# Optimization experiments

Measured on AMD Instinct MI355X. Metric: run time of the kernel, lower is better.

The kernel has to match this reference:

```python
import jax, jax.numpy as jnp
import numpy as np

DIM = 768
HEADS = 12
HIDDEN = int(DIM * 4.0)


def layernorm(x, w, b, eps=1e-5):
    mu = jnp.mean(x, axis=-1, keepdims=True)
    var = jnp.var(x, axis=-1, keepdims=True)
    return (x - mu) * jax.lax.rsqrt(var + eps) * w + b


def setup_inputs() -> dict:
    key = jax.random.key(0)
    ks = jax.random.split(key, 16)
    B, Nq, Nc, D = 4, 1024, 1024, DIM
    s = 0.02
    return {
        "query_tokens": jax.random.normal(ks[0], (B, Nq, D), jnp.float32),
        "context_tokens": jax.random.normal(ks[1], (B, Nc, D), jnp.float32),
        "wind_bias": jax.random.normal(ks[2], (B, 1, Nq, Nc), jnp.float32),
        "ln_q_w": jnp.ones((D,), jnp.float32), "ln_q_b": jnp.zeros((D,), jnp.float32),
        "ln_kv_w": jnp.ones((D,), jnp.float32), "ln_kv_b": jnp.zeros((D,), jnp.float32),
        "Wq": jax.random.normal(ks[3], (D, D), jnp.float32) * s, "bq": jnp.zeros((D,), jnp.float32),
        "Wk": jax.random.normal(ks[4], (D, D), jnp.float32) * s, "bk": jnp.zeros((D,), jnp.float32),
        "Wv": jax.random.normal(ks[5], (D, D), jnp.float32) * s, "bv": jnp.zeros((D,), jnp.float32),
        "Wo": jax.random.normal(ks[6], (D, D), jnp.float32) * s, "bo": jnp.zeros((D,), jnp.float32),
        "beta": jnp.ones((HEADS, 1, 1), jnp.float32),
        "ln_f_w": jnp.ones((D,), jnp.float32), "ln_f_b": jnp.zeros((D,), jnp.float32),
        "W1": jax.random.normal(ks[7], (D, HIDDEN), jnp.float32) * s, "b1": jnp.zeros((HIDDEN,), jnp.float32),
        "W2": jax.random.normal(ks[8], (HIDDEN, D), jnp.float32) * s, "b2": jnp.zeros((D,), jnp.float32),
    }


def reference(query_tokens, context_tokens, wind_bias,
              ln_q_w, ln_q_b, ln_kv_w, ln_kv_b,
              Wq, bq, Wk, bk, Wv, bv, Wo, bo, beta,
              ln_f_w, ln_f_b, W1, b1, W2, b2):
    B, Nq, D = query_tokens.shape
    H = HEADS
    hd = D // H
    scale = hd ** -0.5

    q = layernorm(query_tokens, ln_q_w, ln_q_b) @ Wq + bq
    kv = layernorm(context_tokens, ln_kv_w, ln_kv_b)
    k = kv @ Wk + bk
    v = kv @ Wv + bv

    # [B, H, N, hd]
    q = q.reshape(B, Nq, H, hd).transpose(0, 2, 1, 3)
    k = k.reshape(B, -1, H, hd).transpose(0, 2, 1, 3)
    v = v.reshape(B, -1, H, hd).transpose(0, 2, 1, 3)

    attn = jnp.einsum('bhqd,bhkd->bhqk', q * scale, k)
    attn = attn + beta * wind_bias  # beta: [H,1,1] broadcasts over [B,H,Nq,Nc]
    attn = jax.nn.softmax(attn.astype(jnp.float32), axis=-1).astype(q.dtype)

    out = jnp.einsum('bhqk,bhkd->bhqd', attn, v).transpose(0, 2, 1, 3).reshape(B, Nq, D)
    out = out @ Wo + bo

    x = query_tokens + out
    h = layernorm(x, ln_f_w, ln_f_b)
    h = jax.nn.gelu(h @ W1 + b1, approximate=False) @ W2 + b2
    return x + h
```

## Files before the change

### kernel.cpp

```cpp
#include <hip/hip_runtime.h>
#include <hip/hip_bf16.h>


#define DIM 768
#define HID 3072
#define NHEAD 12
#define BATCH 4
#define SEQ 1024
#define ROWS (BATCH * SEQ)
#define HD 64

typedef __attribute__((ext_vector_type(8))) __bf16 bf16x8;
typedef __attribute__((ext_vector_type(4))) float f32x4;
typedef __attribute__((ext_vector_type(4))) unsigned int u32x4;
typedef __attribute__((ext_vector_type(2))) unsigned int u32x2;

#define MFMA16(a, b, c) __builtin_amdgcn_mfma_f32_16x16x32_bf16((a), (b), (c), 0, 0, 0)

#define GLDS16(g, l)                                                         \
  __builtin_amdgcn_global_load_lds(                                          \
      (const __attribute__((address_space(1))) void*)(g),                    \
      (__attribute__((address_space(3))) void*)(l), 16, 0, 0)

__device__ __forceinline__ unsigned pk2(float lo, float hi) {
  unsigned a = __bfloat16_as_ushort(__float2bfloat16(lo));
  unsigned b = __bfloat16_as_ushort(__float2bfloat16(hi));
  return a | (b << 16);
}

__global__ __launch_bounds__(256) void wg_transpose4(const float* __restrict__ Wq,
                                                     const float* __restrict__ Wk,
                                                     const float* __restrict__ Wv,
                                                     const float* __restrict__ Wo,
                                                     __hip_bfloat16* __restrict__ WqT,
                                                     __hip_bfloat16* __restrict__ WkT,
                                                     __hip_bfloat16* __restrict__ WvT,
                                                     __hip_bfloat16* __restrict__ WoT) {
  __shared__ float tile[32][33];
  const int z = blockIdx.z;
  const float* W = (z == 0) ? Wq : (z == 1) ? Wk : (z == 2) ? Wv : Wo;
  __hip_bfloat16* WT = (z == 0) ? WqT : (z == 1) ? WkT : (z == 2) ? WvT : WoT;
  const int tx = threadIdx.x & 31, ty = threadIdx.x >> 5;
  const int n0 = blockIdx.x * 32, k0 = blockIdx.y * 32;
#pragma unroll
  for (int i = 0; i < 4; i++)
    tile[ty + i * 8][tx] = W[(size_t)(k0 + ty + i * 8) * DIM + n0 + tx];
  __syncthreads();
#pragma unroll
  for (int i = 0; i < 4; i++)
    WT[(size_t)(n0 + ty + i * 8) * DIM + k0 + tx] = __float2bfloat16(tile[tx][ty + i * 8]);
}

__global__ __launch_bounds__(256) void wg_transpose(const float* __restrict__ W,
                                                    __hip_bfloat16* __restrict__ WT,
                                                    int K, int N) {
  __shared__ float tile[32][33];
  const int tx = threadIdx.x & 31, ty = threadIdx.x >> 5;
  const int n0 = blockIdx.x * 32, k0 = blockIdx.y * 32;
#pragma unroll
  for (int i = 0; i < 4; i++)
    tile[ty + i * 8][tx] = W[(size_t)(k0 + ty + i * 8) * N + n0 + tx];
  __syncthreads();
#pragma unroll
  for (int i = 0; i < 4; i++)
    WT[(size_t)(n0 + ty + i * 8) * K + k0 + tx] = __float2bfloat16(tile[tx][ty + i * 8]);
}

__global__ void wg_bcat(const float* __restrict__ bq, const float* __restrict__ bk,
                        const float* __restrict__ bv, float* __restrict__ bc) {
  int i = blockIdx.x * 256 + threadIdx.x;
  if (i < 768) bc[i] = bq[i];
  else if (i < 1536) bc[i] = bk[i - 768];
  else if (i < 2304) bc[i] = bv[i - 1536];
}

template <int DUAL>
__global__ __launch_bounds__(256) void wg_ln(const float* __restrict__ inA,
                                             const float* __restrict__ wA,
                                             const float* __restrict__ bA,
                                             const float* __restrict__ inB,
                                             const float* __restrict__ wB,
                                             const float* __restrict__ bB,
                                             __hip_bfloat16* __restrict__ outbuf) {
  int row = blockIdx.x;
  int t = threadIdx.x;
  const float* in = inA;
  const float* w = wA;
  const float* b = bA;
  int lrow = row;
  if (DUAL && row >= ROWS) {
    in = inB; w = wB; b = bB; lrow = row - ROWS;
  }
  const float* p = in + (size_t)lrow * DIM;
  float v0 = p[t], v1 = p[t + 256], v2 = p[t + 512];
  float s = v0 + v1 + v2;
  float q = v0 * v0 + v1 * v1 + v2 * v2;
#pragma unroll
  for (int d = 1; d < 64; d <<= 1) {
    s += __shfl_xor(s, d);
    q += __shfl_xor(q, d);
  }
  __shared__ float ss[4], sq[4];
  if ((t & 63) == 0) {
    ss[t >> 6] = s;
    sq[t >> 6] = q;
  }
  __syncthreads();
  s = ss[0] + ss[1] + ss[2] + ss[3];
  q = sq[0] + sq[1] + sq[2] + sq[3];
  float mu = s * (1.0f / DIM);
  float var = q * (1.0f / DIM) - mu * mu;
  float rs = rsqrtf(var + 1e-5f);
  __hip_bfloat16* o = outbuf + (size_t)row * DIM;
  o[t] = __float2bfloat16((v0 - mu) * rs * w[t] + b[t]);
  o[t + 256] = __float2bfloat16((v1 - mu) * rs * w[t + 256] + b[t + 256]);
  o[t + 512] = __float2bfloat16((v2 - mu) * rs * w[t + 512] + b[t + 512]);
}

template <int MODE>
__global__ __launch_bounds__(512) void wg_gemm(const __hip_bfloat16* __restrict__ A,
                                               const __hip_bfloat16* __restrict__ BT,
                                               const float* __restrict__ bias,
                                               void* __restrict__ Cout,
                                               const float* __restrict__ resid,
                                               float* __restrict__ aux,
                                               int N, int Kloop, int Kstride, float p0) {
  __shared__ __hip_bfloat16 As[3][128 * 32];
  __shared__ __hip_bfloat16 Bs[3][128 * 32];
  const int t = threadIdx.x;
  const int lane = t & 63;
  const int wave = t >> 6;
  const int wr = wave >> 1, wc = wave & 1;
  const int lhi = lane >> 4, llo = lane & 15;
  const int nbn = N >> 7;
  const int bm = blockIdx.x / nbn, bn = blockIdx.x % nbn;
  const int koff = (MODE == 7) ? blockIdx.y * Kloop : 0;

  const __hip_bfloat16* Ause = A;
  if (MODE == 6 && bn >= 6) Ause = A + (size_t)ROWS * DIM;

  const int srow = t >> 2;
  const int sg = ((t & 3) ^ ((srow >> 1) & 3)) * 8;
  const __hip_bfloat16* Ag = Ause + (size_t)(bm * 128 + srow) * Kstride + koff + sg;
  const __hip_bfloat16* Bg = BT + (size_t)(bn * 128 + srow) * Kstride + koff + sg;

  f32x4 zero = {0.f, 0.f, 0.f, 0.f};
  f32x4 acc[2][4];
#pragma unroll
  for (int i = 0; i < 2; i++)
#pragma unroll
    for (int j = 0; j < 4; j++) acc[i][j] = zero;

  const int nk = Kloop >> 5;

  GLDS16(Ag, &As[0][t * 8]);
  GLDS16(Bg, &Bs[0][t * 8]);
  GLDS16(Ag + 32, &As[1][t * 8]);
  GLDS16(Bg + 32, &Bs[1][t * 8]);

  int buf = 0;
  for (int kt = 0; kt < nk; kt++) {
    if (kt < nk - 1) {
      asm volatile("s_waitcnt vmcnt(2)" ::: "memory");
    } else {
      asm volatile("s_waitcnt vmcnt(0)" ::: "memory");
    }
    __builtin_amdgcn_s_barrier();
    asm volatile("" ::: "memory");
    if (kt + 2 < nk) {
      int nbuf = buf + 2;
      if (nbuf >= 3) nbuf -= 3;
      GLDS16(Ag + (kt + 2) * 32, &As[nbuf][t * 8]);
      GLDS16(Bg + (kt + 2) * 32, &Bs[nbuf][t * 8]);
    }
    bf16x8 af[2], bfr[4];
#pragma unroll
    for (int i = 0; i < 2; i++) {
      const int row = wr * 32 + i * 16 + llo;
      af[i] = *reinterpret_cast<const bf16x8*>(
          &As[buf][row * 32 + ((lhi ^ ((row >> 1) & 3)) << 3)]);
    }
#pragma unroll
    for (int j = 0; j < 4; j++) {
      const int row = wc * 64 + j * 16 + llo;
      bfr[j] = *reinterpret_cast<const bf16x8*>(
          &Bs[buf][row * 32 + ((lhi ^ ((row >> 1) & 3)) << 3)]);
    }
    __builtin_amdgcn_s_setprio(1);
#pragma unroll
    for (int i = 0; i < 2; i++)
#pragma unroll
      for (int j = 0; j < 4; j++) acc[i][j] = MFMA16(af[i], bfr[j], acc[i][j]);
    __builtin_amdgcn_s_setprio(0);
    buf++;
    if (buf == 3) buf = 0;
  }

#pragma unroll
  for (int i = 0; i < 2; i++) {
    int gr = bm * 128 + wr * 32 + i * 16 + lhi * 4;
#pragma unroll
    for (int j = 0; j < 4; j++) {
      int gc = bn * 128 + wc * 64 + j * 16 + llo;
      float bv_ = (MODE == 7) ? 0.f : bias[gc];
#pragma unroll
      for (int r = 0; r < 4; r++) {
        float v = acc[i][j][r] + bv_;
        int row = gr + r;
        size_t idx = (size_t)row * N + gc;
        if (MODE == 3) {
          aux[idx] = resid[idx] + v;
        } else if (MODE == 4) {
          float x3 = v * v * v;
          float z = -2.302208f * v - 0.102943f * x3;
          float g = v / (1.0f + exp2f(z));
          ((__hip_bfloat16*)Cout)[idx] = __float2bfloat16(g);
        } else if (MODE == 7) {
          aux[(size_t)blockIdx.y * ROWS * N + idx] = v;
        } else if (MODE == 6) {
          int sec = gc / 768;
          int n2 = gc - sec * 768;
          __hip_bfloat16* base = (__hip_bfloat16*)Cout;
          if (sec == 0) {
            base[(size_t)row * DIM + n2] = __float2bfloat16(v * p0);
          } else if (sec == 1) {
            base[(size_t)ROWS * DIM + (size_t)row * DIM + n2] = __float2bfloat16(v);
          } else {
            int b_ = row >> 10, n_ = row & 1023;
            int h_ = n2 >> 6, d_ = n2 & 63;
            base[(size_t)2 * ROWS * DIM +
                 (((size_t)(b_ * NHEAD + h_) * HD + d_) << 10) + n_] = __float2bfloat16(v);
          }
        }
      }
    }
  }
}

template <int NP>
__global__ __launch_bounds__(256) void wg_red(const float* __restrict__ partial,
                                              const float* __restrict__ resid,
                                              const float* __restrict__ bias,
                                              float* __restrict__ out) {
  const int i = blockIdx.x * 256 + threadIdx.x;
  const int NF4 = ROWS * DIM / 4;
  if (i >= NF4) return;
  const f32x4* P = (const f32x4*)partial;
  f32x4 p = P[i];
#pragma unroll
  for (int c = 1; c < NP; c++) p += P[i + c * NF4];
  f32x4 r = ((const f32x4*)resid)[i];
  f32x4 bv = ((const f32x4*)bias)[i % (DIM / 4)];
  ((f32x4*)out)[i] = r + p + bv;
}

__global__ __launch_bounds__(256) void wg_attn4(const __hip_bfloat16* __restrict__ Q,
                                                const __hip_bfloat16* __restrict__ Kb,
                                                const __hip_bfloat16* __restrict__ Vt,
                                                const float* __restrict__ wb,
                                                const float* __restrict__ beta,
                                                __hip_bfloat16* __restrict__ O) {
  __shared__ __hip_bfloat16 Ks[2][4096];
  __shared__ __hip_bfloat16 Vs[2][4096];
  const int t = threadIdx.x;
  const int lane = t & 63;
  const int lhi = lane >> 4, llo = lane & 15;

  const int bid = blockIdx.x;
  const int wid = (bid & 7) * 96 + (bid >> 3);
  const int h = wid % NHEAD;
  const int g = wid / NHEAD;
  const int qt = g & 15;
  const int b = g >> 4;
  const float betah = beta[h] * 1.44269504089f;

  const int w = t >> 6;
  const size_t qrow0 = (size_t)b * SEQ + qt * 64 + w * 16;
  const __hip_bfloat16* Qp = Q + qrow0 * DIM + h * HD;
  bf16x8 a0 = *reinterpret_cast<const bf16x8*>(&Qp[(size_t)llo * DIM + lhi * 8]);
  bf16x8 a1 = *reinterpret_cast<const bf16x8*>(&Qp[(size_t)llo * DIM + 32 + lhi * 8]);

  const __hip_bfloat16* Kg = Kb + (size_t)b * SEQ * DIM + h * HD;
  const __hip_bfloat16* Vg = Vt + (size_t)(b * NHEAD + h) * HD * SEQ;
  const float* wrow = wb + (qrow0 + llo) * SEQ;

  const int slot0 = t, slot1 = t + 256;
  const int r0 = slot0 >> 3, c0 = (slot0 & 7) ^ (r0 & 7);
  const int r1 = slot1 >> 3, c1 = (slot1 & 7) ^ (r1 & 7);

  auto stage = [&](int buf, int kb) {
    GLDS16(Kg + (size_t)(kb + r0) * DIM + c0 * 8, &Ks[buf][slot0 * 8]);
    GLDS16(Kg + (size_t)(kb + r1) * DIM + c1 * 8, &Ks[buf][slot1 * 8]);
    GLDS16(Vg + (size_t)r0 * SEQ + kb + c0 * 8, &Vs[buf][slot0 * 8]);
    GLDS16(Vg + (size_t)r1 * SEQ + kb + c1 * 8, &Vs[buf][slot1 * 8]);
  };

  f32x4 zero = {0.f, 0.f, 0.f, 0.f};
  f32x4 oc[4];
#pragma unroll
  for (int c = 0; c < 4; c++) oc[c] = zero;
  float m_ = -1e30f, l_ = 0.f;

  f32x4 wv[4];
#pragma unroll
  for (int c2 = 0; c2 < 4; c2++)
    wv[c2] = *reinterpret_cast<const f32x4*>(&wrow[c2 * 16 + lhi * 4]);

  stage(0, 0);
  __syncthreads();
  int cur = 0;

  const int srcA = (lane & 15) | ((lane & 16) << 1);
  const bool chi = (lane & 32) != 0;

  for (int kt = 0; kt < SEQ / 64; kt++) {
    const int kb = kt * 64;
    f32x4 wvn[4];
    if (kt < SEQ / 64 - 1) {
      stage(cur ^ 1, kb + 64);
#pragma unroll
      for (int c2 = 0; c2 < 4; c2++)
        wvn[c2] = *reinterpret_cast<const f32x4*>(&wrow[kb + 64 + c2 * 16 + lhi * 4]);
    }

    f32x4 sv[4];
    __builtin_amdgcn_s_setprio(1);
#pragma unroll
    for (int c2 = 0; c2 < 4; c2++) {
      const int row = c2 * 16 + llo;
      bf16x8 k0 = *reinterpret_cast<const bf16x8*>(
          &Ks[cur][((row << 3) + (lhi ^ (row & 7))) << 3]);
      bf16x8 k1 = *reinterpret_cast<const bf16x8*>(
          &Ks[cur][((row << 3) + ((4 + lhi) ^ (row & 7))) << 3]);
      f32x4 s_ = zero;
      s_ = MFMA16(k0, a0, s_);
      s_ = MFMA16(k1, a1, s_);
      sv[c2] = s_;
    }
    __builtin_amdgcn_s_setprio(0);

#pragma unroll
    for (int c2 = 0; c2 < 4; c2++)
#pragma unroll
      for (int r = 0; r < 4; r++) sv[c2][r] += betah * wv[c2][r];

    float mx;
    {
      f32x4 m4;
#pragma unroll
      for (int r = 0; r < 4; r++)
        m4[r] = fmaxf(fmaxf(sv[0][r], sv[1][r]), fmaxf(sv[2][r], sv[3][r]));
      mx = fmaxf(fmaxf(m4[0], m4[1]), fmaxf(m4[2], m4[3]));
      mx = fmaxf(mx, __shfl_xor(mx, 16));
      mx = fmaxf(mx, __shfl_xor(mx, 32));
    }

    const bool grow = __any(mx > m_);
    float corr = 1.f;
    if (grow) {
      float mn = fmaxf(m_, mx);
      corr = exp2f(m_ - mn);
      m_ = mn;
    }

#pragma unroll
    for (int c2 = 0; c2 < 4; c2++)
#pragma unroll
      for (int r = 0; r < 4; r++) sv[c2][r] = exp2f(sv[c2][r] - m_);
    f32x4 s4;
#pragma unroll
    for (int r = 0; r < 4; r++) s4[r] = (sv[0][r] + sv[1][r]) + (sv[2][r] + sv[3][r]);
    float rs = (s4[0] + s4[1]) + (s4[2] + s4[3]);
    rs += __shfl_xor(rs, 16);
    rs += __shfl_xor(rs, 32);
    l_ = l_ * corr + rs;

    if (grow) {
      float cr[4];
#pragma unroll
      for (int r = 0; r < 4; r++) cr[r] = __shfl(corr, lhi * 4 + r);
#pragma unroll
      for (int c = 0; c < 4; c++)
#pragma unroll
        for (int r = 0; r < 4; r++) oc[c][r] *= cr[r];
    }

    unsigned p01[4], p23[4];
#pragma unroll
    for (int c2 = 0; c2 < 4; c2++) {
      p01[c2] = pk2(sv[c2][0], sv[c2][1]);
      p23[c2] = pk2(sv[c2][2], sv[c2][3]);
    }
    unsigned a01_0A = (unsigned)__shfl((int)p01[0], srcA);
    unsigned a01_1A = (unsigned)__shfl((int)p01[1], srcA);
    unsigned a23_0A = (unsigned)__shfl((int)p23[0], srcA);
    unsigned a23_1A = (unsigned)__shfl((int)p23[1], srcA);
    unsigned a01_0B = (unsigned)__shfl((int)p01[0], srcA + 16);
    unsigned a01_1B = (unsigned)__shfl((int)p01[1], srcA + 16);
    unsigned a23_0B = (unsigned)__shfl((int)p23[0], srcA + 16);
    unsigned a23_1B = (unsigned)__shfl((int)p23[1], srcA + 16);
    unsigned b01_2A = (unsigned)__shfl((int)p01[2], srcA);
    unsigned b01_3A = (unsigned)__shfl((int)p01[3], srcA);
    unsigned b23_2A = (unsigned)__shfl((int)p23[2], srcA);
    unsigned b23_3A = (unsigned)__shfl((int)p23[3], srcA);
    unsigned b01_2B = (unsigned)__shfl((int)p01[2], srcA + 16);
    unsigned b01_3B = (unsigned)__shfl((int)p01[3], srcA + 16);
    unsigned b23_2B = (unsigned)__shfl((int)p23[2], srcA + 16);
    unsigned b23_3B = (unsigned)__shfl((int)p23[3], srcA + 16);
    u32x4 t0, t1;
    t0[0] = chi ? a01_1A : a01_0A;
    t0[1] = chi ? a23_1A : a23_0A;
    t0[2] = chi ? a01_1B : a01_0B;
    t0[3] = chi ? a23_1B : a23_0B;
    t1[0] = chi ? b01_3A : b01_2A;
    t1[1] = chi ? b23_3A : b23_2A;
    t1[2] = chi ? b01_3B : b01_2B;
    t1[3] = chi ? b23_3B : b23_2B;
    bf16x8 pf0 = __builtin_bit_cast(bf16x8, t0);
    bf16x8 pf1 = __builtin_bit_cast(bf16x8, t1);

    __builtin_amdgcn_s_setprio(1);
#pragma unroll
    for (int c = 0; c < 4; c++) {
      const int row = c * 16 + llo;
      bf16x8 v0 = *reinterpret_cast<const bf16x8*>(
          &Vs[cur][((row << 3) + (lhi ^ (row & 7))) << 3]);
      bf16x8 v1 = *reinterpret_cast<const bf16x8*>(
          &Vs[cur][((row << 3) + ((4 + lhi) ^ (row & 7))) << 3]);
      oc[c] = MFMA16(pf0, v0, oc[c]);
      oc[c] = MFMA16(pf1, v1, oc[c]);
    }
    __builtin_amdgcn_s_setprio(0);

    if (kt < SEQ / 64 - 1) {
#pragma unroll
      for (int c2 = 0; c2 < 4; c2++) wv[c2] = wvn[c2];
    }
    __syncthreads();
    cur ^= 1;
  }

  float iv[4];
  float invl = 1.0f / l_;
#pragma unroll
  for (int r = 0; r < 4; r++) iv[r] = __shfl(invl, lhi * 4 + r);
  __hip_bfloat16* Op = O + qrow0 * DIM + h * HD;
#pragma unroll
  for (int c = 0; c < 4; c++)
#pragma unroll
    for (int r = 0; r < 4; r++)
      Op[(size_t)(lhi * 4 + r) * DIM + c * 16 + llo] = __float2bfloat16(oc[c][r] * iv[r]);
}

extern "C" void kernel_launch(void* const* d_in, const int* in_sizes, int n_in,
                              void* d_out, int out_size, void* d_ws, size_t ws_size,
                              hipStream_t stream) {
  const float* query = (const float*)d_in[0];
  const float* context = (const float*)d_in[1];
  const float* wind = (const float*)d_in[2];
  const float* ln_q_w = (const float*)d_in[3];
  const float* ln_q_b = (const float*)d_in[4];
  const float* ln_kv_w = (const float*)d_in[5];
  const float* ln_kv_b = (const float*)d_in[6];
  const float* Wq = (const float*)d_in[7];
  const float* bq = (const float*)d_in[8];
  const float* Wk = (const float*)d_in[9];
  const float* bk = (const float*)d_in[10];
  const float* Wv = (const float*)d_in[11];
  const float* bv = (const float*)d_in[12];
  const float* Wo = (const float*)d_in[13];
  const float* bo = (const float*)d_in[14];
  const float* beta = (const float*)d_in[15];
  const float* ln_f_w = (const float*)d_in[16];
  const float* ln_f_b = (const float*)d_in[17];
  const float* W1 = (const float*)d_in[18];
  const float* b1 = (const float*)d_in[19];
  const float* W2 = (const float*)d_in[20];
  const float* b2 = (const float*)d_in[21];
  float* out = (float*)d_out;

  char* ws = (char*)d_ws;
  size_t off = 0;
  auto take = [&](size_t bytes) -> char* {
    char* p = ws + off;
    off += (bytes + 255) & ~(size_t)255;
    return p;
  };
  const size_t actB = (size_t)ROWS * DIM * 2;
  __hip_bfloat16* qln = (__hip_bfloat16*)take(actB);
  __hip_bfloat16* kvln = (__hip_bfloat16*)take(actB);
  __hip_bfloat16* qb = (__hip_bfloat16*)take(actB);
  __hip_bfloat16* kbuf = (__hip_bfloat16*)take(actB);
  __hip_bfloat16* vt = (__hip_bfloat16*)take(actB);
  __hip_bfloat16* aout = (__hip_bfloat16*)take(actB);
  __hip_bfloat16* hbuf = (__hip_bfloat16*)take(actB);
  float* xbuf = (float*)take((size_t)ROWS * DIM * 4);
  __hip_bfloat16* hid = (__hip_bfloat16*)take((size_t)ROWS * HID * 2);
  __hip_bfloat16* WqT = (__hip_bfloat16*)take((size_t)DIM * DIM * 2);
  __hip_bfloat16* WkT = (__hip_bfloat16*)take((size_t)DIM * DIM * 2);
  __hip_bfloat16* WvT = (__hip_bfloat16*)take((size_t)DIM * DIM * 2);
  __hip_bfloat16* WoT = (__hip_bfloat16*)take((size_t)DIM * DIM * 2);
  __hip_bfloat16* W1T = (__hip_bfloat16*)take((size_t)DIM * HID * 2);
  __hip_bfloat16* W2T = (__hip_bfloat16*)take((size_t)HID * DIM * 2);
  float* bcat = (float*)take(2304 * 4);
  float* kpart = (float*)take((size_t)4 * ROWS * DIM * 4);

  wg_transpose4<<<dim3(24, 24, 4), 256, 0, stream>>>(Wq, Wk, Wv, Wo, WqT, WkT, WvT, WoT);
  wg_transpose<<<dim3(96, 24), 256, 0, stream>>>(W1, W1T, DIM, HID);
  wg_transpose<<<dim3(24, 96), 256, 0, stream>>>(W2, W2T, HID, DIM);
  wg_bcat<<<9, 256, 0, stream>>>(bq, bk, bv, bcat);

  wg_ln<1><<<2 * ROWS, 256, 0, stream>>>(query, ln_q_w, ln_q_b,
                                         context, ln_kv_w, ln_kv_b, qln);

  const float scale = 0.125f * 1.44269504089f;
  wg_gemm<6><<<32 * 18, 512, 0, stream>>>(qln, WqT, bcat, qb, nullptr, nullptr,
                                          2304, DIM, DIM, scale);

  wg_attn4<<<768, 256, 0, stream>>>(qb, kbuf, vt, wind, beta, aout);

  const int g768 = (ROWS / 128) * (DIM / 128);
  const int g3072 = (ROWS / 128) * (HID / 128);
  wg_gemm<3><<<g768, 512, 0, stream>>>(aout, WoT, bo, nullptr, query, xbuf, DIM, DIM, DIM, 0.f);
  wg_ln<0><<<ROWS, 256, 0, stream>>>(xbuf, ln_f_w, ln_f_b, nullptr, nullptr, nullptr, hbuf);
  wg_gemm<4><<<g3072, 512, 0, stream>>>(hbuf, W1T, b1, hid, nullptr, nullptr, HID, DIM, DIM, 0.f);
  wg_gemm<7><<<dim3(g768, 4), 512, 0, stream>>>(hid, W2T, nullptr, nullptr, nullptr, kpart,
                                                DIM, HID / 4, HID, 0.f);
  wg_red<4><<<(ROWS * DIM / 4 + 255) / 256, 256, 0, stream>>>(kpart, xbuf, b2, out);
}
```

Measured before the change: 215.4 us.

## Widen attention KV tile to 128 and restage V per tile; drop bias concat kernel

The attention kernel now processes 128 keys per iteration instead of 64. It double-buffers K, loads V into a single buffer within the same iteration, and waits on it with an explicit vmcnt and barrier right before the PV MFMAs, so V loading overlaps the QK and softmax work. This halves the loop trip count and per-iteration sync and softmax bookkeeping, at the cost of more LDS use and more registers for the scores and bias values. Separately, the bias concatenation kernel is removed and the QKV GEMM picks bq, bk or bv directly by section, saving one small launch.

```diff
diff --git a/kernel.cpp b/kernel.cpp
--- a/kernel.cpp
+++ b/kernel.cpp
@@ -13,7 +13,6 @@
 typedef __attribute__((ext_vector_type(8))) __bf16 bf16x8;
 typedef __attribute__((ext_vector_type(4))) float f32x4;
 typedef __attribute__((ext_vector_type(4))) unsigned int u32x4;
-typedef __attribute__((ext_vector_type(2))) unsigned int u32x2;
 
 #define MFMA16(a, b, c) __builtin_amdgcn_mfma_f32_16x16x32_bf16((a), (b), (c), 0, 0, 0)
 
@@ -64,14 +63,6 @@
 #pragma unroll
   for (int i = 0; i < 4; i++)
     WT[(size_t)(n0 + ty + i * 8) * K + k0 + tx] = __float2bfloat16(tile[tx][ty + i * 8]);
-}
-
-__global__ void wg_bcat(const float* __restrict__ bq, const float* __restrict__ bk,
-                        const float* __restrict__ bv, float* __restrict__ bc) {
-  int i = blockIdx.x * 256 + threadIdx.x;
-  if (i < 768) bc[i] = bq[i];
-  else if (i < 1536) bc[i] = bk[i - 768];
-  else if (i < 2304) bc[i] = bv[i - 1536];
 }
 
 template <int DUAL>
@@ -202,10 +193,21 @@
 #pragma unroll
     for (int j = 0; j < 4; j++) {
       int gc = bn * 128 + wc * 64 + j * 16 + llo;
-      float bv_ = (MODE == 7) ? 0.f : bias[gc];
+      int sec = 0, n2 = gc;
+      float bval;
+      if (MODE == 6) {
+        sec = gc / 768;
+        n2 = gc - sec * 768;
+        const float* bp = (sec == 0) ? bias : (sec == 1) ? resid : (const float*)aux;
+        bval = bp[n2];
+      } else if (MODE == 7) {
+        bval = 0.f;
+      } else {
+        bval = bias[gc];
+      }
 #pragma unroll
       for (int r = 0; r < 4; r++) {
-        float v = acc[i][j][r] + bv_;
+        float v = acc[i][j][r] + bval;
         int row = gr + r;
         size_t idx = (size_t)row * N + gc;
         if (MODE == 3) {
@@ -218,8 +220,6 @@
         } else if (MODE == 7) {
           aux[(size_t)blockIdx.y * ROWS * N + idx] = v;
         } else if (MODE == 6) {
-          int sec = gc / 768;
-          int n2 = gc - sec * 768;
           __hip_bfloat16* base = (__hip_bfloat16*)Cout;
           if (sec == 0) {
             base[(size_t)row * DIM + n2] = __float2bfloat16(v * p0);
@@ -254,14 +254,14 @@
   ((f32x4*)out)[i] = r + p + bv;
 }
 
-__global__ __launch_bounds__(256) void wg_attn4(const __hip_bfloat16* __restrict__ Q,
+__global__ __launch_bounds__(256) void wg_attn9(const __hip_bfloat16* __restrict__ Q,
                                                 const __hip_bfloat16* __restrict__ Kb,
                                                 const __hip_bfloat16* __restrict__ Vt,
                                                 const float* __restrict__ wb,
                                                 const float* __restrict__ beta,
                                                 __hip_bfloat16* __restrict__ O) {
-  __shared__ __hip_bfloat16 Ks[2][4096];
-  __shared__ __hip_bfloat16 Vs[2][4096];
+  __shared__ __hip_bfloat16 Ks[2][8192];
+  __shared__ __hip_bfloat16 Vs[8192];
   const int t = threadIdx.x;
   const int lane = t & 63;
   const int lhi = lane >> 4, llo = lane & 15;
@@ -284,15 +284,23 @@
   const __hip_bfloat16* Vg = Vt + (size_t)(b * NHEAD + h) * HD * SEQ;
   const float* wrow = wb + (qrow0 + llo) * SEQ;
 
-  const int slot0 = t, slot1 = t + 256;
-  const int r0 = slot0 >> 3, c0 = (slot0 & 7) ^ (r0 & 7);
-  const int r1 = slot1 >> 3, c1 = (slot1 & 7) ^ (r1 & 7);
-
-  auto stage = [&](int buf, int kb) {
-    GLDS16(Kg + (size_t)(kb + r0) * DIM + c0 * 8, &Ks[buf][slot0 * 8]);
-    GLDS16(Kg + (size_t)(kb + r1) * DIM + c1 * 8, &Ks[buf][slot1 * 8]);
-    GLDS16(Vg + (size_t)r0 * SEQ + kb + c0 * 8, &Vs[buf][slot0 * 8]);
-    GLDS16(Vg + (size_t)r1 * SEQ + kb + c1 * 8, &Vs[buf][slot1 * 8]);
+  auto stageK = [&](int buf, int kb) {
+#pragma unroll
+    for (int i = 0; i < 4; i++) {
+      const int s = t + 256 * i;
+      const int row = s >> 3;
+      const int ch = (s & 7) ^ (row & 7);
+      GLDS16(Kg + (size_t)(kb + row) * DIM + ch * 8, &Ks[buf][s * 8]);
+    }
+  };
+  auto stageV = [&](int kb) {
+#pragma unroll
+    for (int i = 0; i < 4; i++) {
+      const int s = t + 256 * i;
+      const int row = s >> 4;
+      const int ch = (s & 8) | ((s & 7) ^ (row & 7));
+      GLDS16(Vg + (size_t)row * SEQ + kb + ch * 8, &Vs[s * 8]);
+    }
   };
 
   f32x4 zero = {0.f, 0.f, 0.f, 0.f};
@@ -301,32 +309,26 @@
   for (int c = 0; c < 4; c++) oc[c] = zero;
   float m_ = -1e30f, l_ = 0.f;
 
-  f32x4 wv[4];
-#pragma unroll
-  for (int c2 = 0; c2 < 4; c2++)
-    wv[c2] = *reinterpret_cast<const f32x4*>(&wrow[c2 * 16 + lhi * 4]);
-
-  stage(0, 0);
+  const int srcA = (lane & 15) | ((lane & 16) << 1);
+  const bool chi = (lane & 32) != 0;
+
+  stageK(0, 0);
   __syncthreads();
   int cur = 0;
 
-  const int srcA = (lane & 15) | ((lane & 16) << 1);
-  const bool chi = (lane & 32) != 0;
-
-  for (int kt = 0; kt < SEQ / 64; kt++) {
-    const int kb = kt * 64;
-    f32x4 wvn[4];
-    if (kt < SEQ / 64 - 1) {
-      stage(cur ^ 1, kb + 64);
-#pragma unroll
-      for (int c2 = 0; c2 < 4; c2++)
-        wvn[c2] = *reinterpret_cast<const f32x4*>(&wrow[kb + 64 + c2 * 16 + lhi * 4]);
-    }
-
-    f32x4 sv[4];
+  for (int kt = 0; kt < 8; kt++) {
+    const int kb = kt * 128;
+    f32x4 wv[8];
+#pragma unroll
+    for (int j = 0; j < 8; j++)
+      wv[j] = *reinterpret_cast<const f32x4*>(&wrow[kb + j * 16 + lhi * 4]);
+    stageV(kb);
+    if (kt < 7) stageK(cur ^ 1, kb + 128);
+
+    f32x4 sv[8];
     __builtin_amdgcn_s_setprio(1);
 #pragma unroll
-    for (int c2 = 0; c2 < 4; c2++) {
+    for (int c2 = 0; c2 < 8; c2++) {
       const int row = c2 * 16 + llo;
       bf16x8 k0 = *reinterpret_cast<const bf16x8*>(
           &Ks[cur][((row << 3) + (lhi ^ (row & 7))) << 3]);
@@ -340,7 +342,7 @@
     __builtin_amdgcn_s_setprio(0);
 
 #pragma unroll
-    for (int c2 = 0; c2 < 4; c2++)
+    for (int c2 = 0; c2 < 8; c2++)
 #pragma unroll
       for (int r = 0; r < 4; r++) sv[c2][r] += betah * wv[c2][r];
 
@@ -348,8 +350,11 @@
     {
       f32x4 m4;
 #pragma unroll
-      for (int r = 0; r < 4; r++)
-        m4[r] = fmaxf(fmaxf(sv[0][r], sv[1][r]), fmaxf(sv[2][r], sv[3][r]));
+      for (int r = 0; r < 4; r++) {
+        float a_ = fmaxf(fmaxf(sv[0][r], sv[1][r]), fmaxf(sv[2][r], sv[3][r]));
+        float b_ = fmaxf(fmaxf(sv[4][r], sv[5][r]), fmaxf(sv[6][r], sv[7][r]));
+        m4[r] = fmaxf(a_, b_);
+      }
       mx = fmaxf(fmaxf(m4[0], m4[1]), fmaxf(m4[2], m4[3]));
       mx = fmaxf(mx, __shfl_xor(mx, 16));
       mx = fmaxf(mx, __shfl_xor(mx, 32));
@@ -363,14 +368,15 @@
       m_ = mn;
     }
 
-#pragma unroll
-    for (int c2 = 0; c2 < 4; c2++)
-#pragma unroll
-      for (int r = 0; r < 4; r++) sv[c2][r] = exp2f(sv[c2][r] - m_);
-    f32x4 s4;
-#pragma unroll
-    for (int r = 0; r < 4; r++) s4[r] = (sv[0][r] + sv[1][r]) + (sv[2][r] + sv[3][r]);
-    float rs = (s4[0] + s4[1]) + (s4[2] + s4[3]);
+    float rs = 0.f;
+#pragma unroll
+    for (int c2 = 0; c2 < 8; c2++) {
+#pragma unroll
+      for (int r = 0; r < 4; r++) {
+        sv[c2][r] = exp2f(sv[c2][r] - m_);
+        rs += sv[c2][r];
+      }
+    }
     rs += __shfl_xor(rs, 16);
     rs += __shfl_xor(rs, 32);
     l_ = l_ * corr + rs;
@@ -385,57 +391,71 @@
         for (int r = 0; r < 4; r++) oc[c][r] *= cr[r];
     }
 
-    unsigned p01[4], p23[4];
-#pragma unroll
-    for (int c2 = 0; c2 < 4; c2++) {
-      p01[c2] = pk2(sv[c2][0], sv[c2][1]);
-      p23[c2] = pk2(sv[c2][2], sv[c2][3]);
-    }
-    unsigned a01_0A = (unsigned)__shfl((int)p01[0], srcA);
-    unsigned a01_1A = (unsigned)__shfl((int)p01[1], srcA);
-    unsigned a23_0A = (unsigned)__shfl((int)p23[0], srcA);
-    unsigned a23_1A = (unsigned)__shfl((int)p23[1], srcA);
-    unsigned a01_0B = (unsigned)__shfl((int)p01[0], srcA + 16);
-    unsigned a01_1B = (unsigned)__shfl((int)p01[1], srcA + 16);
-    unsigned a23_0B = (unsigned)__shfl((int)p23[0], srcA + 16);
-    unsigned a23_1B = (unsigned)__shfl((int)p23[1], srcA + 16);
-    unsigned b01_2A = (unsigned)__shfl((int)p01[2], srcA);
-    unsigned b01_3A = (unsigned)__shfl((int)p01[3], srcA);
-    unsigned b23_2A = (unsigned)__shfl((int)p23[2], srcA);
-    unsigned b23_3A = (unsigned)__shfl((int)p23[3], srcA);
-    unsigned b01_2B = (unsigned)__shfl((int)p01[2], srcA + 16);
-    unsigned b01_3B = (unsigned)__shfl((int)p01[3], srcA + 16);
-    unsigned b23_2B = (unsigned)__shfl((int)p23[2], srcA + 16);
-    unsigned b23_3B = (unsigned)__shfl((int)p23[3], srcA + 16);
-    u32x4 t0, t1;
-    t0[0] = chi ? a01_1A : a01_0A;
-    t0[1] = chi ? a23_1A : a23_0A;
-    t0[2] = chi ? a01_1B : a01_0B;
-    t0[3] = chi ? a23_1B : a23_0B;
-    t1[0] = chi ? b01_3A : b01_2A;
-    t1[1] = chi ? b23_3A : b23_2A;
-    t1[2] = chi ? b01_3B : b01_2B;
-    t1[3] = chi ? b23_3B : b23_2B;
-    bf16x8 pf0 = __builtin_bit_cast(bf16x8, t0);
-    bf16x8 pf1 = __builtin_bit_cast(bf16x8, t1);
+    bf16x8 pf[4];
+#pragma unroll
+    for (int hf = 0; hf < 2; hf++) {
+      unsigned p01[4], p23[4];
+#pragma unroll
+      for (int c2 = 0; c2 < 4; c2++) {
+        p01[c2] = pk2(sv[hf * 4 + c2][0], sv[hf * 4 + c2][1]);
+        p23[c2] = pk2(sv[hf * 4 + c2][2], sv[hf * 4 + c2][3]);
+      }
+      unsigned a01_0A = (unsigned)__shfl((int)p01[0], srcA);
+      unsigned a01_1A = (unsigned)__shfl((int)p01[1], srcA);
+      unsigned a23_0A = (unsigned)__shfl((int)p23[0], srcA);
+      unsigned a23_1A = (unsigned)__shfl((int)p23[1], srcA);
+      unsigned a01_0B = (unsigned)__shfl((int)p01[0], srcA + 16);
+      unsigned a01_1B = (unsigned)__shfl((int)p01[1], srcA + 16);
+      unsigned a23_0B = (unsigned)__shfl((int)p23[0], srcA + 16);
+      unsigned a23_1B = (unsigned)__shfl((int)p23[1], srcA + 16);
+      unsigned b01_2A = (unsigned)__shfl((int)p01[2], srcA);
+      unsigned b01_3A = (unsigned)__shfl((int)p01[3], srcA);
+      unsigned b23_2A = (unsigned)__shfl((int)p23[2], srcA);
+      unsigned b23_3A = (unsigned)__shfl((int)p23[3], srcA);
+      unsigned b01_2B = (unsigned)__shfl((int)p01[2], srcA + 16);
+      unsigned b01_3B = (unsigned)__shfl((int)p01[3], srcA + 16);
+      unsigned b23_2B = (unsigned)__shfl((int)p23[2], srcA + 16);
+      unsigned b23_3B = (unsigned)__shfl((int)p23[3], srcA + 16);
+      u32x4 t0, t1;
+      t0[0] = chi ? a01_1A : a01_0A;
+      t0[1] = chi ? a23_1A : a23_0A;
+      t0[2] = chi ? a01_1B : a01_0B;
+      t0[3] = chi ? a23_1B : a23_0B;
+      t1[0] = chi ? b01_3A : b01_2A;
+      t1[1] = chi ? b23_3A : b23_2A;
+      t1[2] = chi ? b01_3B : b01_2B;
+      t1[3] = chi ? b23_3B : b23_2B;
+      pf[hf * 2 + 0] = __builtin_bit_cast(bf16x8, t0);
+      pf[hf * 2 + 1] = __builtin_bit_cast(bf16x8, t1);
+    }
+
+    if (kt < 7) {
+      asm volatile("s_waitcnt vmcnt(4)" ::: "memory");
+    } else {
+      asm volatile("s_waitcnt vmcnt(0)" ::: "memory");
+    }
+    __builtin_amdgcn_s_barrier();
+    __builtin_amdgcn_sched_barrier(0);
 
     __builtin_amdgcn_s_setprio(1);
 #pragma unroll
     for (int c = 0; c < 4; c++) {
       const int row = c * 16 + llo;
-      bf16x8 v0 = *reinterpret_cast<const bf16x8*>(
-          &Vs[cur][((row << 3) + (lhi ^ (row & 7))) << 3]);
-      bf16x8 v1 = *reinterpret_cast<const bf16x8*>(
-          &Vs[cur][((row << 3) + ((4 + lhi) ^ (row & 7))) << 3]);
-      oc[c] = MFMA16(pf0, v0, oc[c]);
-      oc[c] = MFMA16(pf1, v1, oc[c]);
+      bf16x8 v00 = *reinterpret_cast<const bf16x8*>(
+          &Vs[((row << 4) + (lhi ^ (row & 7))) << 3]);
+      bf16x8 v01 = *reinterpret_cast<const bf16x8*>(
+          &Vs[((row << 4) + ((4 + lhi) ^ (row & 7))) << 3]);
+      oc[c] = MFMA16(pf[0], v00, oc[c]);
+      oc[c] = MFMA16(pf[1], v01, oc[c]);
+      bf16x8 v10 = *reinterpret_cast<const bf16x8*>(
+          &Vs[((row << 4) + (8 | (lhi ^ (row & 7)))) << 3]);
+      bf16x8 v11 = *reinterpret_cast<const bf16x8*>(
+          &Vs[((row << 4) + (8 | ((4 + lhi) ^ (row & 7)))) << 3]);
+      oc[c] = MFMA16(pf[2], v10, oc[c]);
+      oc[c] = MFMA16(pf[3], v11, oc[c]);
     }
     __builtin_amdgcn_s_setprio(0);
 
-    if (kt < SEQ / 64 - 1) {
-#pragma unroll
-      for (int c2 = 0; c2 < 4; c2++) wv[c2] = wvn[c2];
-    }
     __syncthreads();
     cur ^= 1;
   }
@@ -502,22 +522,20 @@
   __hip_bfloat16* WoT = (__hip_bfloat16*)take((size_t)DIM * DIM * 2);
   __hip_bfloat16* W1T = (__hip_bfloat16*)take((size_t)DIM * HID * 2);
   __hip_bfloat16* W2T = (__hip_bfloat16*)take((size_t)HID * DIM * 2);
-  float* bcat = (float*)take(2304 * 4);
   float* kpart = (float*)take((size_t)4 * ROWS * DIM * 4);
 
   wg_transpose4<<<dim3(24, 24, 4), 256, 0, stream>>>(Wq, Wk, Wv, Wo, WqT, WkT, WvT, WoT);
   wg_transpose<<<dim3(96, 24), 256, 0, stream>>>(W1, W1T, DIM, HID);
   wg_transpose<<<dim3(24, 96), 256, 0, stream>>>(W2, W2T, HID, DIM);
-  wg_bcat<<<9, 256, 0, stream>>>(bq, bk, bv, bcat);
 
   wg_ln<1><<<2 * ROWS, 256, 0, stream>>>(query, ln_q_w, ln_q_b,
                                          context, ln_kv_w, ln_kv_b, qln);
 
   const float scale = 0.125f * 1.44269504089f;
-  wg_gemm<6><<<32 * 18, 512, 0, stream>>>(qln, WqT, bcat, qb, nullptr, nullptr,
+  wg_gemm<6><<<32 * 18, 512, 0, stream>>>(qln, WqT, bq, qb, bk, (float*)bv,
                                           2304, DIM, DIM, scale);
 
-  wg_attn4<<<768, 256, 0, stream>>>(qb, kbuf, vt, wind, beta, aout);
+  wg_attn9<<<768, 256, 0, stream>>>(qb, kbuf, vt, wind, beta, aout);
 
   const int g768 = (ROWS / 128) * (DIM / 128);
   const int g3072 = (ROWS / 128) * (HID / 128);
```

Result: slower. 229.9 us (+6.7%).
